# Kernel tuning notes

Measured on AMD Instinct MI355X. Metric: run time of the kernel, lower is better.

Reference implementation:

```python
import jax, jax.numpy as jnp
import numpy as np


def _rope(x):
    # x: [..., T, hs]
    T, hs = x.shape[-2], x.shape[-1]
    pos = jnp.arange(T, dtype=x.dtype)[:, None]                      # [T,1]
    theta = 1.0 / (10000.0 ** (jnp.arange(0, hs, 2, dtype=x.dtype) / hs))  # [hs/2]
    ang = pos * theta                                                # [T, hs/2]
    cos, sin = jnp.cos(ang), jnp.sin(ang)
    x1, x2 = x[..., 0::2], x[..., 1::2]
    out = jnp.stack([x1 * cos - x2 * sin, x1 * sin + x2 * cos], axis=-1)
    return out.reshape(x.shape)


def _layernorm(x, w, b, eps=1e-5):
    mu = jnp.mean(x, axis=-1, keepdims=True)
    var = jnp.mean(jnp.square(x - mu), axis=-1, keepdims=True)
    return (x - mu) * jax.lax.rsqrt(var + eps) * w + b


def setup_inputs() -> dict:
    key = jax.random.key(0)
    ks = jax.random.split(key, 8)
    B, T, D, H, HS = 8, 1024, 1024, 16, 64
    s = lambda fan: 1.0 / np.sqrt(fan)
    return {
        'x': jax.random.normal(ks[0], (B, T, D), jnp.float32),
        'wq': jax.random.normal(ks[1], (H, D, HS), jnp.float32) * s(D),
        'wk': jax.random.normal(ks[2], (H, D, HS), jnp.float32) * s(D),
        'wv': jax.random.normal(ks[3], (H, D, HS), jnp.float32) * s(D),
        'w_proj': jax.random.normal(ks[4], (D, D), jnp.float32) * s(D),
        'b_proj': jnp.zeros((D,), jnp.float32),
        'ln1_w': jnp.ones((D,), jnp.float32),
        'ln1_b': jnp.zeros((D,), jnp.float32),
        'ln2_w': jnp.ones((D,), jnp.float32),
        'ln2_b': jnp.zeros((D,), jnp.float32),
        'w1': jax.random.normal(ks[5], (D, 4 * D), jnp.float32) * s(D),
        'b1': jnp.zeros((4 * D,), jnp.float32),
        'w2': jax.random.normal(ks[6], (4 * D, D), jnp.float32) * s(4 * D),
        'b2': jnp.zeros((D,), jnp.float32),
    }


def reference(x, wq, wk, wv, w_proj, b_proj, ln1_w, ln1_b, ln2_w, ln2_b, w1, b1, w2, b2):
    B, T, D = x.shape
    H, _, HS = wq.shape
    # --- attention sub-block (pre-LN, causal, RoPE on q/k) ---
    xn = _layernorm(x, ln1_w, ln1_b)
    q = jnp.einsum('btd,hdk->bhtk', xn, wq)   # [B,H,T,HS]
    k = jnp.einsum('btd,hdk->bhtk', xn, wk)
    v = jnp.einsum('btd,hdk->bhtk', xn, wv)
    q = _rope(q)
    k = _rope(k)
    scores = jnp.einsum('bhqk,bhsk->bhqs', q, k) * (HS ** -0.5)  # [B,H,T,T]
    causal = jnp.tril(jnp.ones((T, T), bool))
    scores = jnp.where(causal, scores, -jnp.inf)
    attn = jax.nn.softmax(scores, axis=-1)
    o = jnp.einsum('bhqs,bhsk->bhqk', attn, v)                   # [B,H,T,HS]
    o = jnp.transpose(o, (0, 2, 1, 3)).reshape(B, T, H * HS)     # concat heads
    x = x + o @ w_proj + b_proj                                  # dropout is identity in eval
    # --- FFN sub-block ---
    xn2 = _layernorm(x, ln2_w, ln2_b)
    h = jax.nn.relu(xn2 @ w1 + b1)
    x = x + h @ w2 + b2
    return x
```

## Files before the change

### kernel.cpp

```cpp
#include <hip/hip_runtime.h>
#include <hip/hip_bf16.h>
#include <math.h>

#define DEV static __device__ __forceinline__

typedef __attribute__((ext_vector_type(8))) __bf16 bf16x8;
typedef __attribute__((ext_vector_type(4))) float f32x4;
typedef __attribute__((ext_vector_type(8))) unsigned short ushort8;
typedef __attribute__((ext_vector_type(4))) unsigned short ushort4v;

#define Bb 8
#define Tt 1024
#define Dd 1024
#define Hh 16
#define HS 64
#define BT 8192
#define DFF 4096
#define QS 8388608ull

DEV unsigned short f2bf(float f) {
  union { float f; unsigned int u; } v; v.f = f;
  unsigned int r = v.u + 0x7fffu + ((v.u >> 16) & 1u);
  return (unsigned short)(r >> 16);
}
DEV float bf2f(unsigned short h) {
  union { unsigned int u; float f; } v; v.u = ((unsigned int)h) << 16;
  return v.f;
}

DEV void gload_lds16(const void* g, void* l) {
  __builtin_amdgcn_global_load_lds(
      (const __attribute__((address_space(1))) void*)g,
      (__attribute__((address_space(3))) void*)l, 16, 0, 0);
}

__global__ void rope_tab_k(float2* __restrict__ tab) {
  int idx = blockIdx.x * 256 + threadIdx.x;
  int t = idx >> 5, i = idx & 31;
  float theta = exp2f(-(float)i * (13.287712379549449f / 32.f));
  float sn, cs;
  sincosf((float)t * theta, &sn, &cs);
  tab[idx] = make_float2(cs, sn);
}

__global__ __launch_bounds__(256) void pack_qkv_t(const float* __restrict__ wq,
                                                  const float* __restrict__ wk,
                                                  const float* __restrict__ wv,
                                                  unsigned short* __restrict__ dst) {
  __shared__ float tile[32][33];
  int z = blockIdx.z, which = z >> 4, hh = z & 15;
  const float* src = which == 0 ? wq : (which == 1 ? wk : wv);
  int d0 = blockIdx.y * 32, hs0 = blockIdx.x * 32;
  int c = threadIdx.x & 31, r8 = threadIdx.x >> 5;
  #pragma unroll
  for (int r = 0; r < 4; ++r) {
    int d = d0 + r8 + r * 8;
    tile[r8 + r * 8][c] = src[((size_t)hh * Dd + d) * HS + hs0 + c];
  }
  __syncthreads();
  #pragma unroll
  for (int r = 0; r < 4; ++r) {
    int hs = hs0 + r8 + r * 8;
    dst[((size_t)which * 1024 + hh * 64 + hs) * Dd + d0 + c] = f2bf(tile[c][r8 + r * 8]);
  }
}

__global__ __launch_bounds__(256) void pack_t_tiled(const float* __restrict__ src,
                                                    unsigned short* __restrict__ dst,
                                                    int N, int K) {
  __shared__ float tile[32][33];
  int n0 = blockIdx.x * 32, k0 = blockIdx.y * 32;
  int c = threadIdx.x & 31, r8 = threadIdx.x >> 5;
  #pragma unroll
  for (int r = 0; r < 4; ++r)
    tile[r8 + r * 8][c] = src[(size_t)(k0 + r8 + r * 8) * N + n0 + c];
  __syncthreads();
  #pragma unroll
  for (int r = 0; r < 4; ++r)
    dst[(size_t)(n0 + r8 + r * 8) * K + k0 + c] = f2bf(tile[c][r8 + r * 8]);
}

__global__ __launch_bounds__(256) void ln_k(const float* __restrict__ in,
                                            const float* __restrict__ w,
                                            const float* __restrict__ b,
                                            unsigned short* __restrict__ out) {
  __shared__ float sbuf[8];
  int row = blockIdx.x, t = threadIdx.x;
  const float4 v = ((const float4*)(in + (size_t)row * Dd))[t];
  float s = v.x + v.y + v.z + v.w;
  float q = v.x * v.x + v.y * v.y + v.z * v.z + v.w * v.w;
  #pragma unroll
  for (int o = 32; o > 0; o >>= 1) { s += __shfl_down(s, o); q += __shfl_down(q, o); }
  if ((t & 63) == 0) { sbuf[t >> 6] = s; sbuf[4 + (t >> 6)] = q; }
  __syncthreads();
  s = (sbuf[0] + sbuf[1]) + (sbuf[2] + sbuf[3]);
  q = (sbuf[4] + sbuf[5]) + (sbuf[6] + sbuf[7]);
  float mu = s * (1.f / Dd);
  float var = q * (1.f / Dd) - mu * mu;
  float inv = rsqrtf(var + 1e-5f);
  const float4 wv = ((const float4*)w)[t];
  const float4 bv = ((const float4*)b)[t];
  ushort4v r;
  r[0] = f2bf((v.x - mu) * inv * wv.x + bv.x);
  r[1] = f2bf((v.y - mu) * inv * wv.y + bv.y);
  r[2] = f2bf((v.z - mu) * inv * wv.z + bv.z);
  r[3] = f2bf((v.w - mu) * inv * wv.w + bv.w);
  *(ushort4v*)&out[(size_t)row * Dd + t * 4] = r;
}

DEV void stage64(const unsigned short* __restrict__ g, int ldK, int k0,
                 unsigned short* lds, int tid) {
  #pragma unroll
  for (int j = 0; j < 4; ++j) {
    int idx = j * 256 + tid;
    int r = idx >> 3, slot = idx & 7;
    gload_lds16(g + (size_t)r * ldK + k0 + ((slot ^ (r & 7)) * 8),
                lds + (size_t)idx * 8);
  }
}

template <int MODE>
__global__ __launch_bounds__(256) void gemm_bk64(
    const unsigned short* __restrict__ A, const unsigned short* __restrict__ Bt,
    int M, int N, int K,
    const float* __restrict__ bias, const float* __restrict__ resid,
    float* __restrict__ outf, unsigned short* __restrict__ outb) {
  __shared__ __align__(16) unsigned short As[2][128 * 64];
  __shared__ __align__(16) unsigned short Bs[2][128 * 64];
  const int tid = threadIdx.x;
  const int lane = tid & 63, wave = tid >> 6;
  const int l15 = lane & 15, lg = lane >> 4;
  const int wm = wave >> 1, wn = wave & 1;
  const int sw = l15 & 7;

  int nwg = gridDim.x * gridDim.y;
  int orig = blockIdx.y * gridDim.x + blockIdx.x;
  int swz = (orig & 7) * (nwg >> 3) + (orig >> 3);
  int bx = swz % gridDim.x, by = swz / gridDim.x;
  const int brow = by * 128, bcol = bx * 128;

  const unsigned short* Ag = A + (size_t)brow * K;
  const unsigned short* Bg = Bt + (size_t)bcol * K;
  const int NT = K >> 6;

  stage64(Ag, K, 0, As[0], tid);
  stage64(Bg, K, 0, Bs[0], tid);
  asm volatile("s_waitcnt vmcnt(0)" ::: "memory");
  __builtin_amdgcn_s_barrier();

  f32x4 acc[4][4] = {};

  for (int t = 0; t < NT; ++t) {
    const unsigned short* Abuf = As[t & 1];
    const unsigned short* Bbuf = Bs[t & 1];
    if (t + 1 < NT) {
      stage64(Ag, K, (t + 1) * 64, As[(t + 1) & 1], tid);
      stage64(Bg, K, (t + 1) * 64, Bs[(t + 1) & 1], tid);
    }
    bf16x8 af[4][2], bf[4][2];
    #pragma unroll
    for (int mi = 0; mi < 4; ++mi) {
      int lr = wm * 64 + mi * 16 + l15;
      #pragma unroll
      for (int kk = 0; kk < 2; ++kk)
        af[mi][kk] = *(const bf16x8*)&Abuf[(size_t)lr * 64 + (((kk * 4 + lg) ^ sw) * 8)];
    }
    #pragma unroll
    for (int ni = 0; ni < 4; ++ni) {
      int lr = wn * 64 + ni * 16 + l15;
      #pragma unroll
      for (int kk = 0; kk < 2; ++kk)
        bf[ni][kk] = *(const bf16x8*)&Bbuf[(size_t)lr * 64 + (((kk * 4 + lg) ^ sw) * 8)];
    }
    asm volatile("s_waitcnt lgkmcnt(0)" ::: "memory");
    __builtin_amdgcn_sched_barrier(0);
    __builtin_amdgcn_s_setprio(1);
    #pragma unroll
    for (int kk = 0; kk < 2; ++kk)
      #pragma unroll
      for (int mi = 0; mi < 4; ++mi)
        #pragma unroll
        for (int ni = 0; ni < 4; ++ni)
          acc[mi][ni] = __builtin_amdgcn_mfma_f32_16x16x32_bf16(af[mi][kk], bf[ni][kk], acc[mi][ni], 0, 0, 0);
    __builtin_amdgcn_s_setprio(0);
    if (t + 1 < NT) asm volatile("s_waitcnt vmcnt(0)" ::: "memory");
    __builtin_amdgcn_s_barrier();
  }

  #pragma unroll
  for (int m = 0; m < 4; ++m) {
    #pragma unroll
    for (int n = 0; n < 4; ++n) {
      int row0 = brow + wm * 64 + m * 16 + lg * 4;
      int col = bcol + wn * 64 + n * 16 + l15;
      if constexpr (MODE == 0) {
        int b = row0 >> 10, t0 = row0 & 1023;
        int which = col >> 10, rem = col & 1023, hh = rem >> 6, hs = rem & 63;
        if (which == 2) {
          uint2 pk;
          pk.x = (unsigned int)f2bf(acc[m][n][0]) | ((unsigned int)f2bf(acc[m][n][1]) << 16);
          pk.y = (unsigned int)f2bf(acc[m][n][2]) | ((unsigned int)f2bf(acc[m][n][3]) << 16);
          *(uint2*)&outb[2 * QS + ((size_t)(b * Hh + hh) * HS + hs) * Tt + t0] = pk;
        } else {
          const float2* tab = (const float2*)bias;
          float qs = (which == 0) ? 0.18033688f : 1.0f;
          float sgn = ((hs & 1) == 0) ? -1.0f : 1.0f;
          #pragma unroll
          for (int r = 0; r < 4; ++r) {
            float own = acc[m][n][r];
            float partner = __shfl_xor(own, 1);
            float2 cssn = tab[(size_t)(t0 + r) * 32 + (hs >> 1)];
            float val = (cssn.x * own + sgn * cssn.y * partner) * qs;
            outb[(size_t)which * QS + ((size_t)((b * Hh + hh) * Tt + t0 + r)) * HS + hs] =
                f2bf(val);
          }
        }
      } else if constexpr (MODE == 1) {
        #pragma unroll
        for (int r = 0; r < 4; ++r)
          outf[(size_t)(row0 + r) * N + col] =
              resid[(size_t)(row0 + r) * N + col] + acc[m][n][r] + bias[col];
      } else {
        #pragma unroll
        for (int r = 0; r < 4; ++r) {
          float z = acc[m][n][r] + bias[col];
          outb[(size_t)(row0 + r) * N + col] = f2bf(z > 0.f ? z : 0.f);
        }
      }
    }
  }
}

__global__ __launch_bounds__(256) void attn_k(const unsigned short* __restrict__ qkv,
                                              unsigned short* __restrict__ O) {
  __shared__ __align__(16) unsigned short K_lds[2][64 * 64];
  __shared__ __align__(16) unsigned short Vt_lds[2][64 * 64];
  __shared__ __align__(16) unsigned short P_lds[4][32 * 64];
  const int tid = threadIdx.x;
  const int wave = tid >> 6, lane = tid & 63;
  const int l15 = lane & 15, lg = lane >> 4;
  const int sw = l15 & 7;
  const int bh = blockIdx.x;
  const int q0 = (7 - (int)blockIdx.y) * 128;
  const int qw0 = q0 + wave * 32;

  bf16x8 qf[2][2];
  {
    const unsigned short* Qg = qkv + ((size_t)bh * Tt + qw0 + l15) * HS;
    #pragma unroll
    for (int qi = 0; qi < 2; ++qi)
      #pragma unroll
      for (int dg = 0; dg < 2; ++dg)
        qf[qi][dg] = *(const bf16x8*)&Qg[(size_t)qi * 16 * HS + dg * 32 + lg * 8];
  }
  f32x4 oacc[2][4] = {};
  float m_r[2] = {-1e30f, -1e30f};
  float l_r[2] = {0.f, 0.f};

  const unsigned short* Kg = qkv + QS + (size_t)bh * Tt * HS;
  const unsigned short* Vg = qkv + 2 * QS + (size_t)bh * HS * Tt;

  const int srow = lane >> 3;
  const int scol = ((lane & 7) ^ (srow & 7)) * 8;
  const int i0 = wave * 2, i1 = wave * 2 + 1;

#define STAGE_KV(s0_, buf_)                                                        \
  do {                                                                             \
    gload_lds16(Kg + (size_t)((s0_) + i0 * 8 + srow) * HS + scol,                  \
                (char*)&K_lds[buf_][0] + i0 * 1024);                               \
    gload_lds16(Kg + (size_t)((s0_) + i1 * 8 + srow) * HS + scol,                  \
                (char*)&K_lds[buf_][0] + i1 * 1024);                               \
    gload_lds16(Vg + (size_t)(i0 * 8 + srow) * Tt + (s0_) + scol,                  \
                (char*)&Vt_lds[buf_][0] + i0 * 1024);                              \
    gload_lds16(Vg + (size_t)(i1 * 8 + srow) * Tt + (s0_) + scol,                  \
                (char*)&Vt_lds[buf_][0] + i1 * 1024);                              \
  } while (0)

  const int nsteps = (q0 + 128) >> 6;
  STAGE_KV(0, 0);

  for (int t = 0; t < nsteps; ++t) {
    const int s0 = t << 6;
    if (t + 1 < nsteps) {
      STAGE_KV(s0 + 64, (t + 1) & 1);
      asm volatile("s_waitcnt vmcnt(4)" ::: "memory");
    } else {
      asm volatile("s_waitcnt vmcnt(0)" ::: "memory");
    }
    __builtin_amdgcn_s_barrier();

    const unsigned short* Kb = K_lds[t & 1];
    const unsigned short* Vb = Vt_lds[t & 1];

    if (s0 <= qw0 + 31) {
      f32x4 st[4][2];
      #pragma unroll
      for (int si = 0; si < 4; ++si) {
        bf16x8 kf0 = *(const bf16x8*)&Kb[(size_t)(si * 16 + l15) * 64 + ((lg ^ sw) * 8)];
        bf16x8 kf1 = *(const bf16x8*)&Kb[(size_t)(si * 16 + l15) * 64 + (((4 + lg) ^ sw) * 8)];
        #pragma unroll
        for (int qi = 0; qi < 2; ++qi) {
          f32x4 a = {};
          a = __builtin_amdgcn_mfma_f32_16x16x32_bf16(kf0, qf[qi][0], a, 0, 0, 0);
          a = __builtin_amdgcn_mfma_f32_16x16x32_bf16(kf1, qf[qi][1], a, 0, 0, 0);
          st[si][qi] = a;
        }
      }
      if (s0 + 63 > qw0) {
        #pragma unroll
        for (int si = 0; si < 4; ++si)
          #pragma unroll
          for (int qi = 0; qi < 2; ++qi) {
            int base = (s0 + si * 16 + lg * 4) - (qw0 + qi * 16 + l15);
            #pragma unroll
            for (int r = 0; r < 4; ++r)
              if (base + r > 0) st[si][qi][r] = -1e30f;
          }
      }
      #pragma unroll
      for (int qi = 0; qi < 2; ++qi) {
        float ms[4];
        #pragma unroll
        for (int si = 0; si < 4; ++si)
          ms[si] = fmaxf(fmaxf(st[si][qi][0], st[si][qi][1]),
                         fmaxf(st[si][qi][2], st[si][qi][3]));
        float pm = fmaxf(fmaxf(ms[0], ms[1]), fmaxf(ms[2], ms[3]));
        pm = fmaxf(pm, __shfl_xor(pm, 16));
        pm = fmaxf(pm, __shfl_xor(pm, 32));
        if (__any(pm - m_r[qi] > 8.f)) {
          float mn = fmaxf(m_r[qi], pm);
          float corr = __builtin_amdgcn_exp2f(m_r[qi] - mn);
          m_r[qi] = mn;
          l_r[qi] *= corr;
          #pragma unroll
          for (int r = 0; r < 4; ++r) {
            float c = __shfl(corr, (lane & 48) + lg * 4 + r);
            #pragma unroll
            for (int dj = 0; dj < 4; ++dj) oacc[qi][dj][r] *= c;
          }
        }
        float rs = 0.f;
        #pragma unroll
        for (int si = 0; si < 4; ++si) {
          #pragma unroll
          for (int r = 0; r < 4; ++r) {
            float p = __builtin_amdgcn_exp2f(st[si][qi][r] - m_r[qi]);
            st[si][qi][r] = p;
            rs += p;
          }
        }
        rs += __shfl_xor(rs, 16);
        rs += __shfl_xor(rs, 32);
        l_r[qi] += rs;
        #pragma unroll
        for (int si = 0; si < 4; ++si) {
          uint2 pk;
          asm("v_cvt_pk_bf16_f32 %0, %1, %2"
              : "=v"(pk.x) : "v"(st[si][qi][0]), "v"(st[si][qi][1]));
          asm("v_cvt_pk_bf16_f32 %0, %1, %2"
              : "=v"(pk.y) : "v"(st[si][qi][2]), "v"(st[si][qi][3]));
          int slot = si * 2 + (lg >> 1);
          *(uint2*)&P_lds[wave][(size_t)(qi * 16 + l15) * 64 + ((slot ^ sw) * 8) + (lg & 1) * 4] = pk;
        }
      }
      bf16x8 pf[2][2];
      #pragma unroll
      for (int qi = 0; qi < 2; ++qi)
        #pragma unroll
        for (int sg = 0; sg < 2; ++sg)
          pf[qi][sg] = *(const bf16x8*)&P_lds[wave][(size_t)(qi * 16 + l15) * 64 + (((sg * 4 + lg) ^ sw) * 8)];
      #pragma unroll
      for (int dj = 0; dj < 4; ++dj) {
        bf16x8 vf0 = *(const bf16x8*)&Vb[(size_t)(dj * 16 + l15) * 64 + ((lg ^ sw) * 8)];
        bf16x8 vf1 = *(const bf16x8*)&Vb[(size_t)(dj * 16 + l15) * 64 + (((4 + lg) ^ sw) * 8)];
        #pragma unroll
        for (int qi = 0; qi < 2; ++qi) {
          oacc[qi][dj] = __builtin_amdgcn_mfma_f32_16x16x32_bf16(pf[qi][0], vf0, oacc[qi][dj], 0, 0, 0);
          oacc[qi][dj] = __builtin_amdgcn_mfma_f32_16x16x32_bf16(pf[qi][1], vf1, oacc[qi][dj], 0, 0, 0);
        }
      }
    }
    __builtin_amdgcn_s_barrier();
  }
#undef STAGE_KV

  int b = bh >> 4, hh = bh & 15;
  #pragma unroll
  for (int qi = 0; qi < 2; ++qi) {
    float linv = 1.f / l_r[qi];
    #pragma unroll
    for (int r = 0; r < 4; ++r) {
      float li = __shfl(linv, (lane & 48) + lg * 4 + r);
      int qg = qw0 + qi * 16 + lg * 4 + r;
      unsigned short* Og = O + ((size_t)(b * Tt + qg)) * Dd + hh * HS;
      #pragma unroll
      for (int dj = 0; dj < 4; ++dj)
        Og[dj * 16 + l15] = f2bf(oacc[qi][dj][r] * li);
    }
  }
}

extern "C" void kernel_launch(void* const* d_in, const int* in_sizes, int n_in,
                              void* d_out, int out_size, void* d_ws, size_t ws_size,
                              hipStream_t stream) {
  const float* x      = (const float*)d_in[0];
  const float* wq     = (const float*)d_in[1];
  const float* wk     = (const float*)d_in[2];
  const float* wv     = (const float*)d_in[3];
  const float* w_proj = (const float*)d_in[4];
  const float* b_proj = (const float*)d_in[5];
  const float* ln1_w  = (const float*)d_in[6];
  const float* ln1_b  = (const float*)d_in[7];
  const float* ln2_w  = (const float*)d_in[8];
  const float* ln2_b  = (const float*)d_in[9];
  const float* w1     = (const float*)d_in[10];
  const float* b1     = (const float*)d_in[11];
  const float* w2     = (const float*)d_in[12];
  const float* b2     = (const float*)d_in[13];
  float* out = (float*)d_out;

  char* ws = (char*)d_ws;
  unsigned short* Wt_qkv  = (unsigned short*)(ws + 0);
  unsigned short* Wt_proj = (unsigned short*)(ws + 6291456);
  unsigned short* Wt_1    = (unsigned short*)(ws + 8388608);
  unsigned short* Wt_2    = (unsigned short*)(ws + 16777216);
  float*          x1      = (float*)(ws + 25165824);
  unsigned short* xn      = (unsigned short*)(ws + 58720256);
  unsigned short* qkv     = (unsigned short*)(ws + 75497472);
  unsigned short* O       = (unsigned short*)(ws + 125829120);
  unsigned short* xn2     = O;
  unsigned short* hbuf    = (unsigned short*)(ws + 58720256);
  float*          rtab    = (float*)(ws + 141557760);

  rope_tab_k<<<128, 256, 0, stream>>>((float2*)rtab);
  pack_qkv_t<<<dim3(2, 32, 48), 256, 0, stream>>>(wq, wk, wv, Wt_qkv);
  pack_t_tiled<<<dim3(32, 32), 256, 0, stream>>>(w_proj, Wt_proj, 1024, 1024);
  pack_t_tiled<<<dim3(128, 32), 256, 0, stream>>>(w1, Wt_1, 4096, 1024);
  pack_t_tiled<<<dim3(32, 128), 256, 0, stream>>>(w2, Wt_2, 1024, 4096);

  ln_k<<<BT, 256, 0, stream>>>(x, ln1_w, ln1_b, xn);

  gemm_bk64<0><<<dim3(24, 64), 256, 0, stream>>>(xn, Wt_qkv, BT, 3072, 1024,
                                                 rtab, nullptr, nullptr, qkv);

  attn_k<<<dim3(128, 8), 256, 0, stream>>>(qkv, O);

  gemm_bk64<1><<<dim3(8, 64), 256, 0, stream>>>(O, Wt_proj, BT, 1024, 1024,
                                                b_proj, x, x1, nullptr);
  ln_k<<<BT, 256, 0, stream>>>(x1, ln2_w, ln2_b, xn2);

  gemm_bk64<2><<<dim3(32, 64), 256, 0, stream>>>(xn2, Wt_1, BT, 4096, 1024,
                                                 b1, nullptr, nullptr, hbuf);
  gemm_bk64<1><<<dim3(8, 64), 256, 0, stream>>>(hbuf, Wt_2, BT, 1024, 4096,
                                                b2, x1, out, nullptr);
}
```

Before: 343.5 us.

## Switch GEMM to BK=32 triple-buffered pipeline with two tiles in flight

The GEMM kernel now uses K-tiles of 32 instead of 64 and a three-stage LDS ring buffer. Two tiles are prefetched ahead, and partial vmcnt waits let the next load overlap the current compute. The LDS layout packs two rows per 64-element line with a new XOR swizzle, and launch bounds ask for 3 blocks per CU to raise occupancy. The cost is half as many MFMAs per barrier and twice as many loop iterations and barriers, so per-iteration sync overhead grows.

New measurement: 368.7 us. +7.3%, slower.

```diff
diff --git a/kernel.cpp b/kernel.cpp
--- a/kernel.cpp
+++ b/kernel.cpp
@@ -108,30 +108,31 @@
   *(ushort4v*)&out[(size_t)row * Dd + t * 4] = r;
 }
 
-DEV void stage64(const unsigned short* __restrict__ g, int ldK, int k0,
+DEV void stage32(const unsigned short* __restrict__ g, int ldK, int k0,
                  unsigned short* lds, int tid) {
   #pragma unroll
-  for (int j = 0; j < 4; ++j) {
+  for (int j = 0; j < 2; ++j) {
     int idx = j * 256 + tid;
-    int r = idx >> 3, slot = idx & 7;
-    gload_lds16(g + (size_t)r * ldK + k0 + ((slot ^ (r & 7)) * 8),
-                lds + (size_t)idx * 8);
+    int R = idx >> 3, s = idx & 7;
+    int L = s ^ (R & 7);
+    int mrow = 2 * R + (L >> 2);
+    int kg = L & 3;
+    gload_lds16(g + (size_t)mrow * ldK + k0 + kg * 8, lds + (size_t)idx * 8);
   }
 }
 
 template <int MODE>
-__global__ __launch_bounds__(256) void gemm_bk64(
+__global__ __launch_bounds__(256, 3) void gemm_bk32(
     const unsigned short* __restrict__ A, const unsigned short* __restrict__ Bt,
     int M, int N, int K,
     const float* __restrict__ bias, const float* __restrict__ resid,
     float* __restrict__ outf, unsigned short* __restrict__ outb) {
-  __shared__ __align__(16) unsigned short As[2][128 * 64];
-  __shared__ __align__(16) unsigned short Bs[2][128 * 64];
+  __shared__ __align__(16) unsigned short As[3][4096];
+  __shared__ __align__(16) unsigned short Bs[3][4096];
   const int tid = threadIdx.x;
   const int lane = tid & 63, wave = tid >> 6;
   const int l15 = lane & 15, lg = lane >> 4;
   const int wm = wave >> 1, wn = wave & 1;
-  const int sw = l15 & 7;
 
   int nwg = gridDim.x * gridDim.y;
   int orig = blockIdx.y * gridDim.x + blockIdx.x;
@@ -141,49 +142,55 @@
 
   const unsigned short* Ag = A + (size_t)brow * K;
   const unsigned short* Bg = Bt + (size_t)bcol * K;
-  const int NT = K >> 6;
-
-  stage64(Ag, K, 0, As[0], tid);
-  stage64(Bg, K, 0, Bs[0], tid);
-  asm volatile("s_waitcnt vmcnt(0)" ::: "memory");
+  const int NT = K >> 5;
+
+  stage32(Ag, K, 0, As[0], tid);
+  stage32(Bg, K, 0, Bs[0], tid);
+  stage32(Ag, K, 32, As[1], tid);
+  stage32(Bg, K, 32, Bs[1], tid);
+  asm volatile("s_waitcnt vmcnt(4)" ::: "memory");
   __builtin_amdgcn_s_barrier();
 
   f32x4 acc[4][4] = {};
 
   for (int t = 0; t < NT; ++t) {
-    const unsigned short* Abuf = As[t & 1];
-    const unsigned short* Bbuf = Bs[t & 1];
-    if (t + 1 < NT) {
-      stage64(Ag, K, (t + 1) * 64, As[(t + 1) & 1], tid);
-      stage64(Bg, K, (t + 1) * 64, Bs[(t + 1) & 1], tid);
-    }
-    bf16x8 af[4][2], bf[4][2];
+    const int cb = t % 3;
+    const unsigned short* Abuf = As[cb];
+    const unsigned short* Bbuf = Bs[cb];
+    if (t + 2 < NT) {
+      const int nb = (t + 2) % 3;
+      stage32(Ag, K, (t + 2) * 32, As[nb], tid);
+      stage32(Bg, K, (t + 2) * 32, Bs[nb], tid);
+    }
+    bf16x8 af[4], bf[4];
     #pragma unroll
     for (int mi = 0; mi < 4; ++mi) {
-      int lr = wm * 64 + mi * 16 + l15;
-      #pragma unroll
-      for (int kk = 0; kk < 2; ++kk)
-        af[mi][kk] = *(const bf16x8*)&Abuf[(size_t)lr * 64 + (((kk * 4 + lg) ^ sw) * 8)];
+      int r = wm * 64 + mi * 16 + l15;
+      int R = r >> 1;
+      int s = ((r & 1) * 4 + lg) ^ (R & 7);
+      af[mi] = *(const bf16x8*)&Abuf[(size_t)R * 64 + s * 8];
     }
     #pragma unroll
     for (int ni = 0; ni < 4; ++ni) {
-      int lr = wn * 64 + ni * 16 + l15;
-      #pragma unroll
-      for (int kk = 0; kk < 2; ++kk)
-        bf[ni][kk] = *(const bf16x8*)&Bbuf[(size_t)lr * 64 + (((kk * 4 + lg) ^ sw) * 8)];
+      int r = wn * 64 + ni * 16 + l15;
+      int R = r >> 1;
+      int s = ((r & 1) * 4 + lg) ^ (R & 7);
+      bf[ni] = *(const bf16x8*)&Bbuf[(size_t)R * 64 + s * 8];
     }
     asm volatile("s_waitcnt lgkmcnt(0)" ::: "memory");
     __builtin_amdgcn_sched_barrier(0);
     __builtin_amdgcn_s_setprio(1);
     #pragma unroll
-    for (int kk = 0; kk < 2; ++kk)
-      #pragma unroll
-      for (int mi = 0; mi < 4; ++mi)
-        #pragma unroll
-        for (int ni = 0; ni < 4; ++ni)
-          acc[mi][ni] = __builtin_amdgcn_mfma_f32_16x16x32_bf16(af[mi][kk], bf[ni][kk], acc[mi][ni], 0, 0, 0);
+    for (int mi = 0; mi < 4; ++mi)
+      #pragma unroll
+      for (int ni = 0; ni < 4; ++ni)
+        acc[mi][ni] = __builtin_amdgcn_mfma_f32_16x16x32_bf16(af[mi], bf[ni], acc[mi][ni], 0, 0, 0);
     __builtin_amdgcn_s_setprio(0);
-    if (t + 1 < NT) asm volatile("s_waitcnt vmcnt(0)" ::: "memory");
+    if (t + 2 < NT) {
+      asm volatile("s_waitcnt vmcnt(4)" ::: "memory");
+    } else if (t + 1 < NT) {
+      asm volatile("s_waitcnt vmcnt(0)" ::: "memory");
+    }
     __builtin_amdgcn_s_barrier();
   }
 
@@ -440,17 +447,17 @@
 
   ln_k<<<BT, 256, 0, stream>>>(x, ln1_w, ln1_b, xn);
 
-  gemm_bk64<0><<<dim3(24, 64), 256, 0, stream>>>(xn, Wt_qkv, BT, 3072, 1024,
+  gemm_bk32<0><<<dim3(24, 64), 256, 0, stream>>>(xn, Wt_qkv, BT, 3072, 1024,
                                                  rtab, nullptr, nullptr, qkv);
 
   attn_k<<<dim3(128, 8), 256, 0, stream>>>(qkv, O);
 
-  gemm_bk64<1><<<dim3(8, 64), 256, 0, stream>>>(O, Wt_proj, BT, 1024, 1024,
+  gemm_bk32<1><<<dim3(8, 64), 256, 0, stream>>>(O, Wt_proj, BT, 1024, 1024,
                                                 b_proj, x, x1, nullptr);
   ln_k<<<BT, 256, 0, stream>>>(x1, ln2_w, ln2_b, xn2);
 
-  gemm_bk64<2><<<dim3(32, 64), 256, 0, stream>>>(xn2, Wt_1, BT, 4096, 1024,
+  gemm_bk32<2><<<dim3(32, 64), 256, 0, stream>>>(xn2, Wt_1, BT, 4096, 1024,
                                                  b1, nullptr, nullptr, hbuf);
-  gemm_bk64<1><<<dim3(8, 64), 256, 0, stream>>>(hbuf, Wt_2, BT, 1024, 4096,
+  gemm_bk32<1><<<dim3(8, 64), 256, 0, stream>>>(hbuf, Wt_2, BT, 1024, 4096,
                                                 b2, x1, out, nullptr);
 }
```
